# Optimization experiments

Hardware: AMD Instinct MI355X
Metric: run time of the kernel (lower is better)

## Reference

```python
import jax, jax.numpy as jnp
import numpy as np

CHANNELS = 64
HIDDEN = 1024
LAYERS = 24
NODE_TYPES = 19
BN_EPS = 1e-5

N_NODES = 200000
N_EDGES = 800000
N_RULES = 50000


def setup_inputs() -> dict:
    key = jax.random.key(0)
    ks = jax.random.split(key, 16)
    nodes = jax.random.randint(ks[0], (N_NODES,), 0, NODE_TYPES)
    sources = jax.random.randint(ks[1], (N_EDGES,), 0, N_NODES)
    targets = jax.random.randint(ks[2], (N_EDGES,), 0, N_NODES)
    rules = jax.random.randint(ks[3], (N_RULES,), 0, N_NODES)
    f32 = jnp.float32
    emb = jax.random.normal(ks[4], (NODE_TYPES, CHANNELS), f32)
    # per-layer, per-direction (out/back) Conv params, stacked [LAYERS, 2, ...]
    W = jax.random.normal(ks[5], (LAYERS, 2, CHANNELS, CHANNELS), f32) * 0.125  # ~xavier
    b = jax.random.normal(ks[6], (LAYERS, 2, CHANNELS), f32) * 0.01
    gamma = 1.0 + 0.1 * jax.random.normal(ks[7], (LAYERS, 2, CHANNELS), f32)
    beta = 0.01 * jax.random.normal(ks[8], (LAYERS, 2, CHANNELS), f32)
    rmean = 0.01 * jax.random.normal(ks[9], (LAYERS, 2, CHANNELS), f32)
    rvar = jax.random.uniform(ks[10], (LAYERS, 2, CHANNELS), f32, 0.5, 1.5)
    Wh = jax.random.normal(ks[11], (HIDDEN, CHANNELS), f32) * 0.05
    bh = jax.random.normal(ks[12], (HIDDEN,), f32) * 0.01
    Wo = jax.random.normal(ks[13], (1, HIDDEN), f32) * 0.03
    return {"nodes": nodes, "sources": sources, "targets": targets, "rules": rules,
            "emb": emb, "W": W, "b": b, "gamma": gamma, "beta": beta,
            "rmean": rmean, "rvar": rvar, "Wh": Wh, "bh": bh, "Wo": Wo}


def reference(nodes, sources, targets, rules, emb, W, b, gamma, beta, rmean, rvar, Wh, bh, Wo):
    n = nodes.shape[0]

    def conv(x, src, tgt, Wi, bi, g, be, rm, rv):
        # scatter_mean of gathered source features onto target nodes
        s = jax.ops.segment_sum(x[src], tgt, num_segments=n)            # [n, C]
        cnt = jax.ops.segment_sum(jnp.ones(src.shape, x.dtype), tgt, num_segments=n)
        m = s / jnp.maximum(cnt, 1.0)[:, None]
        # eval-mode BatchNorm1d (running stats) fused as affine
        xn = (m - rm) * (g * jax.lax.rsqrt(rv + BN_EPS)) + be
        return jax.nn.relu(xn @ Wi.T + bi)

    def layer(x, p):
        Wl, bl, gl, bel, rml, rvl = p
        out = conv(x, sources, targets, Wl[0], bl[0], gl[0], bel[0], rml[0], rvl[0])
        back = conv(x, targets, sources, Wl[1], bl[1], gl[1], bel[1], rml[1], rvl[1])
        return x + out + back, None

    x = emb[nodes]                                                      # [n, C]
    x, _ = jax.lax.scan(layer, x, (W, b, gamma, beta, rmean, rvar))
    h = jax.nn.relu(x[rules] @ Wh.T + bh)                               # [R, HIDDEN]
    return (h @ Wo.T)[:, 0]                                             # [R]
```

## Files before the change

kernel.cpp:

```cpp
#include <hip/hip_runtime.h>

#define N_NODES 200000
#define N_EDGES 800000
#define N_RULES 50000
#define NLAYERS 24
#define SCAN_NB 196
#define RP_STRIDE 200064

typedef short bf16x8 __attribute__((ext_vector_type(8)));
typedef float floatx4 __attribute__((ext_vector_type(4)));

__device__ __forceinline__ unsigned short f2bf(float f) {
  unsigned int b = __float_as_uint(f);
  b += 0x7FFFu + ((b >> 16) & 1u);
  return (unsigned short)(b >> 16);
}
__device__ __forceinline__ float bf2f(unsigned short u) {
  return __uint_as_float(((unsigned int)u) << 16);
}


__global__ void k_hist(const int* __restrict__ src, const int* __restrict__ tgt,
                       int* __restrict__ deg_out, int* __restrict__ deg_back,
                       int* __restrict__ rank_out, int* __restrict__ rank_back) {
  int e = blockIdx.x * 256 + threadIdx.x;
  rank_out[e]  = atomicAdd(&deg_out[tgt[e]], 1);
  rank_back[e] = atomicAdd(&deg_back[src[e]], 1);
}

__global__ void k_scanA(const int* __restrict__ deg, int* __restrict__ part) {
  int y = blockIdx.y;
  const int* d = deg + y * N_NODES;
  __shared__ int sh[256];
  int t = threadIdx.x;
  int base = blockIdx.x * 1024 + t * 4;
  int s = 0;
  #pragma unroll
  for (int k = 0; k < 4; ++k) { int i = base + k; if (i < N_NODES) s += d[i]; }
  sh[t] = s; __syncthreads();
  for (int off = 128; off > 0; off >>= 1) { if (t < off) sh[t] += sh[t + off]; __syncthreads(); }
  if (t == 0) part[y * SCAN_NB + blockIdx.x] = sh[0];
}

__global__ void k_scanB(int* __restrict__ part, int* __restrict__ rp) {
  int y = blockIdx.y;
  __shared__ int buf[256];
  int t = threadIdx.x;
  int v = (t < SCAN_NB) ? part[y * SCAN_NB + t] : 0;
  buf[t] = v; __syncthreads();
  for (int off = 1; off < 256; off <<= 1) {
    int x = (t >= off) ? buf[t - off] : 0;
    __syncthreads();
    buf[t] += x;
    __syncthreads();
  }
  if (t < SCAN_NB) part[y * SCAN_NB + t] = buf[t] - v;
  if (t == 0) rp[y * RP_STRIDE + N_NODES] = N_EDGES;
}

__global__ void k_scanC(const int* __restrict__ deg, const int* __restrict__ part,
                        int* __restrict__ rp) {
  int y = blockIdx.y;
  const int* d = deg + y * N_NODES;
  int* r = rp + y * RP_STRIDE;
  __shared__ int buf[256];
  int t = threadIdx.x;
  int base = blockIdx.x * 1024 + t * 4;
  int dv[4]; int s = 0;
  #pragma unroll
  for (int k = 0; k < 4; ++k) { int i = base + k; dv[k] = (i < N_NODES) ? d[i] : 0; s += dv[k]; }
  buf[t] = s; __syncthreads();
  int sv = s;
  for (int off = 1; off < 256; off <<= 1) {
    int x = (t >= off) ? buf[t - off] : 0;
    __syncthreads();
    buf[t] += x;
    __syncthreads();
  }
  int e = part[y * SCAN_NB + blockIdx.x] + buf[t] - sv;
  #pragma unroll
  for (int k = 0; k < 4; ++k) { int i = base + k; if (i < N_NODES) r[i] = e; e += dv[k]; }
}

__global__ void k_fill(const int* __restrict__ src, const int* __restrict__ tgt,
                       const int* __restrict__ rp_out, const int* __restrict__ rp_back,
                       const int* __restrict__ rank_out, const int* __restrict__ rank_back,
                       int* __restrict__ ci_out, int* __restrict__ ci_back) {
  int e = blockIdx.x * 256 + threadIdx.x;
  int s = src[e], t = tgt[e];
  ci_out[rp_out[t] + rank_out[e]] = s;
  ci_back[rp_back[s] + rank_back[e]] = t;
}

__global__ void k_prep(const float* __restrict__ W, const float* __restrict__ b,
                       const float* __restrict__ gamma, const float* __restrict__ beta,
                       const float* __restrict__ rmean, const float* __restrict__ rvar,
                       unsigned short* __restrict__ WpF, float* __restrict__ bp) {
  int d = blockIdx.x, l = blockIdx.y, lane = threadIdx.x;
  int ld = l * 2 + d;
  __shared__ float s_s[64], t_s[64];
  float s = gamma[ld * 64 + lane] * rsqrtf(rvar[ld * 64 + lane] + 1e-5f);
  s_s[lane] = s;
  t_s[lane] = beta[ld * 64 + lane] - rmean[ld * 64 + lane] * s;
  __syncthreads();
  float bias = b[ld * 64 + lane];
  for (int j = 0; j < 64; ++j) bias += W[(ld * 64 + lane) * 64 + j] * t_s[j];
  bp[ld * 64 + lane] = bias;
  #pragma unroll
  for (int f = 0; f < 8; ++f) {
    int ct = f >> 1, kh = f & 1;
    int row = ct * 16 + (lane & 15);
    #pragma unroll
    for (int jj = 0; jj < 8; ++jj) {
      int k = kh * 32 + (lane >> 4) * 8 + jj;
      float val = W[(ld * 64 + row) * 64 + k] * s_s[k];
      WpF[(ld * 8 + f) * 512 + lane * 8 + jj] = f2bf(val);
    }
  }
}

__global__ void k_prep2(const float* __restrict__ Wh,
                        unsigned short* __restrict__ WhFhi,
                        unsigned short* __restrict__ WhFlo) {
  int jt = blockIdx.x, lane = threadIdx.x;
  #pragma unroll
  for (int kh = 0; kh < 2; ++kh) {
    #pragma unroll
    for (int jj = 0; jj < 8; ++jj) {
      int j = jt * 16 + (lane & 15);
      int k = kh * 32 + (lane >> 4) * 8 + jj;
      float wv = Wh[j * 64 + k];
      unsigned short hi = f2bf(wv);
      WhFhi[(jt * 2 + kh) * 512 + lane * 8 + jj] = hi;
      WhFlo[(jt * 2 + kh) * 512 + lane * 8 + jj] = f2bf(wv - bf2f(hi));
    }
  }
}

__global__ void k_embed(const int* __restrict__ nodes, const float* __restrict__ emb,
                        unsigned short* __restrict__ hi_a,
                        unsigned short* __restrict__ lo) {
  int gid = blockIdx.x * 256 + threadIdx.x;
  int i = gid >> 6, c = gid & 63;
  float v = emb[nodes[i] * 64 + c];
  unsigned short h = f2bf(v);
  hi_a[gid] = h;
  lo[gid] = f2bf(v - bf2f(h));
}

__global__ __launch_bounds__(256, 8) void k_layer(
    const unsigned short* __restrict__ hi_in,
    unsigned short* __restrict__ hi_out,
    unsigned short* __restrict__ lo,
    const int* __restrict__ rp0, const int* __restrict__ ci0,
    const int* __restrict__ rp1, const int* __restrict__ ci1,
    const unsigned short* __restrict__ WfL, const float* __restrict__ bpL) {
  __shared__ __align__(16) unsigned short m_s[4][2][16 * 72];
  __shared__ float bp_s[128];
  int tid = threadIdx.x, lane = tid & 63, w = tid >> 6;
  if (tid < 128) bp_s[tid] = bpL[tid];
  __syncthreads();
  int base = (blockIdx.x * 4 + w) * 16;
  int n15 = lane & 15, q = lane >> 4;

  int rpv0 = (lane < 17) ? rp0[base + lane] : 0;
  int rpv1 = (lane < 17) ? rp1[base + lane] : 0;
  int rs0 = __builtin_amdgcn_readlane(rpv0, 0);
  int re0 = __builtin_amdgcn_readlane(rpv0, 16);
  int rs1 = __builtin_amdgcn_readlane(rpv1, 0);
  int re1 = __builtin_amdgcn_readlane(rpv1, 16);
  int cv0 = (rs0 + lane < re0) ? ci0[rs0 + lane] : 0;
  int cv1 = (rs1 + lane < re1) ? ci1[rs1 + lane] : 0;

  for (int d = 0; d < 2; ++d) {
    const int* ci = d ? ci1 : ci0;
    int rpv = d ? rpv1 : rpv0;
    int rs  = d ? rs1  : rs0;
    int re  = d ? re1  : re0;
    int cv  = d ? cv1  : cv0;
    unsigned short* md = &m_s[w][d][0];
    int cur = 0;
    int cstart = rs;
    int cend = __builtin_amdgcn_readlane(rpv, 1);
    float acc = 0.f;

    for (int cb = rs; cb < re; cb += 64) {
      int ce = (cb + 64 < re) ? cb + 64 : re;
      int cv_next = (cb + 64 + lane < re) ? ci[cb + 64 + lane] : 0;
      for (int j0 = cb; j0 < ce; j0 += 16) {
        float v[16];
        #pragma unroll
        for (int u = 0; u < 16; ++u) {
          int sn = __builtin_amdgcn_readlane(cv, j0 + u - cb);
          v[u] = bf2f(hi_in[sn * 64 + lane]);
        }
        #pragma unroll
        for (int u = 0; u < 16; ++u) {
          int j = j0 + u;
          if (j < ce) {
            while (j >= cend) {
              int deg = cend - cstart;
              float invc = deg > 0 ? __builtin_amdgcn_rcpf((float)deg) : 0.f;
              md[cur * 72 + lane] = f2bf(acc * invc);
              acc = 0.f; cur++; cstart = cend;
              cend = __builtin_amdgcn_readlane(rpv, cur + 1);
            }
            acc += v[u];
          }
        }
      }
      cv = cv_next;
    }
    #pragma unroll 1
    while (cur < 16) {
      int deg = cend - cstart;
      float invc = deg > 0 ? __builtin_amdgcn_rcpf((float)deg) : 0.f;
      md[cur * 72 + lane] = f2bf(acc * invc);
      acc = 0.f; cstart = cend; cur++;
      if (cur < 16) cend = __builtin_amdgcn_readlane(rpv, cur + 1);
    }
  }

  bf16x8 b0d0 = *(const bf16x8*)&m_s[w][0][n15 * 72 + q * 8];
  bf16x8 b1d0 = *(const bf16x8*)&m_s[w][0][n15 * 72 + 32 + q * 8];
  bf16x8 b0d1 = *(const bf16x8*)&m_s[w][1][n15 * 72 + q * 8];
  bf16x8 b1d1 = *(const bf16x8*)&m_s[w][1][n15 * 72 + 32 + q * 8];
  float* ys = (float*)&m_s[w][0][0];
  #pragma unroll
  for (int ct = 0; ct < 4; ++ct) {
    const unsigned short* wf0 = WfL + (ct * 2) * 512 + lane * 8;
    const unsigned short* wf1 = WfL + 4096 + (ct * 2) * 512 + lane * 8;
    floatx4 d40 = {0.f, 0.f, 0.f, 0.f};
    floatx4 d41 = {0.f, 0.f, 0.f, 0.f};
    d40 = __builtin_amdgcn_mfma_f32_16x16x32_bf16(*(const bf16x8*)wf0, b0d0, d40, 0, 0, 0);
    d40 = __builtin_amdgcn_mfma_f32_16x16x32_bf16(*(const bf16x8*)(wf0 + 512), b1d0, d40, 0, 0, 0);
    d41 = __builtin_amdgcn_mfma_f32_16x16x32_bf16(*(const bf16x8*)wf1, b0d1, d41, 0, 0, 0);
    d41 = __builtin_amdgcn_mfma_f32_16x16x32_bf16(*(const bf16x8*)(wf1 + 512), b1d1, d41, 0, 0, 0);
    int c0 = ct * 16 + q * 4;
    floatx4 yv;
    #pragma unroll
    for (int i = 0; i < 4; ++i)
      yv[i] = fmaxf(d40[i] + bp_s[c0 + i], 0.f)
            + fmaxf(d41[i] + bp_s[64 + c0 + i], 0.f);
    *(floatx4*)&ys[n15 * 68 + c0] = yv;
  }

  #pragma unroll
  for (int r = 0; r < 16; ++r) {
    int gi = (base + r) * 64 + lane;
    float xv = bf2f(hi_in[gi]) + bf2f(lo[gi]) + ys[r * 68 + lane];
    unsigned short h = f2bf(xv);
    hi_out[gi] = h;
    lo[gi] = f2bf(xv - bf2f(h));
  }
}

__global__ __launch_bounds__(256) void k_final(
    const unsigned short* __restrict__ hi, const unsigned short* __restrict__ lo,
    const int* __restrict__ rules,
    const unsigned short* __restrict__ WhFhi, const unsigned short* __restrict__ WhFlo,
    const float* __restrict__ bh, const float* __restrict__ Wo,
    float* __restrict__ out) {
  __shared__ __align__(16) float bh_s[1024], wo_s[1024];
  int tid = threadIdx.x, lane = tid & 63, w = tid >> 6;
  ((floatx4*)bh_s)[tid] = ((const floatx4*)bh)[tid];
  ((floatx4*)wo_s)[tid] = ((const floatx4*)Wo)[tid];
  __syncthreads();
  int n15 = lane & 15, q = lane >> 4;
  int rbase = (blockIdx.x * 4 + w) * 16;
  int ru = rbase + n15;
  int nd = rules[ru < N_RULES ? ru : N_RULES - 1];
  bf16x8 b0h = *(const bf16x8*)&hi[nd * 64 + q * 8];
  bf16x8 b1h = *(const bf16x8*)&hi[nd * 64 + 32 + q * 8];
  bf16x8 b0l = *(const bf16x8*)&lo[nd * 64 + q * 8];
  bf16x8 b1l = *(const bf16x8*)&lo[nd * 64 + 32 + q * 8];
  float acc = 0.f;
  #pragma unroll 4
  for (int jt = 0; jt < 64; ++jt) {
    const unsigned short* fh = WhFhi + (jt * 2) * 512 + lane * 8;
    const unsigned short* fl = WhFlo + (jt * 2) * 512 + lane * 8;
    bf16x8 a0h = *(const bf16x8*)fh;
    bf16x8 a1h = *(const bf16x8*)(fh + 512);
    bf16x8 a0l = *(const bf16x8*)fl;
    bf16x8 a1l = *(const bf16x8*)(fl + 512);
    floatx4 d4 = {0.f, 0.f, 0.f, 0.f};
    d4 = __builtin_amdgcn_mfma_f32_16x16x32_bf16(a0h, b0h, d4, 0, 0, 0);
    d4 = __builtin_amdgcn_mfma_f32_16x16x32_bf16(a1h, b1h, d4, 0, 0, 0);
    d4 = __builtin_amdgcn_mfma_f32_16x16x32_bf16(a0h, b0l, d4, 0, 0, 0);
    d4 = __builtin_amdgcn_mfma_f32_16x16x32_bf16(a1h, b1l, d4, 0, 0, 0);
    d4 = __builtin_amdgcn_mfma_f32_16x16x32_bf16(a0l, b0h, d4, 0, 0, 0);
    d4 = __builtin_amdgcn_mfma_f32_16x16x32_bf16(a1l, b1h, d4, 0, 0, 0);
    floatx4 bh4 = *(const floatx4*)&bh_s[jt * 16 + q * 4];
    floatx4 wo4 = *(const floatx4*)&wo_s[jt * 16 + q * 4];
    #pragma unroll
    for (int i = 0; i < 4; ++i)
      acc += fmaxf(d4[i] + bh4[i], 0.f) * wo4[i];
  }
  acc += __shfl_down(acc, 32);
  acc += __shfl_down(acc, 16);
  if (lane < 16 && rbase + lane < N_RULES) out[rbase + lane] = acc;
}

extern "C" void kernel_launch(void* const* d_in, const int* in_sizes, int n_in,
                              void* d_out, int out_size, void* d_ws, size_t ws_size,
                              hipStream_t stream) {
  const int* nodes = (const int*)d_in[0];
  const int* sources = (const int*)d_in[1];
  const int* targets = (const int*)d_in[2];
  const int* rules = (const int*)d_in[3];
  const float* emb = (const float*)d_in[4];
  const float* W = (const float*)d_in[5];
  const float* b = (const float*)d_in[6];
  const float* gamma = (const float*)d_in[7];
  const float* beta = (const float*)d_in[8];
  const float* rmean = (const float*)d_in[9];
  const float* rvar = (const float*)d_in[10];
  const float* Wh = (const float*)d_in[11];
  const float* bh = (const float*)d_in[12];
  const float* Wo = (const float*)d_in[13];
  float* out = (float*)d_out;

  if (ws_size < 95100000u) return;

  char* ws = (char*)d_ws;
  unsigned short* hi_a = (unsigned short*)(ws + 0);
  unsigned short* hi_b = (unsigned short*)(ws + 25600000);
  unsigned short* lo   = (unsigned short*)(ws + 51200000);
  int* deg_out  = (int*)(ws + 76800000);
  int* deg_back = (int*)(ws + 77600000);
  int* rank_out = (int*)(ws + 78400000);
  int* rank_back= (int*)(ws + 81600000);
  int* rp_out   = (int*)(ws + 84800000);
  int* rp_back  = (int*)(ws + 85600256);
  int* ci_out   = (int*)(ws + 86400512);
  int* ci_back  = (int*)(ws + 89600512);
  int* part     = (int*)(ws + 92800512);
  unsigned short* WpF   = (unsigned short*)(ws + 92802080);
  float* bp             = (float*)(ws + 93195296);
  unsigned short* WhFhi = (unsigned short*)(ws + 93207584);
  unsigned short* WhFlo = (unsigned short*)(ws + 93338656);

  (void)hipMemsetAsync(deg_out, 0, 1600000u, stream);

  k_hist<<<3125, 256, 0, stream>>>(sources, targets, deg_out, deg_back,
                                   rank_out, rank_back);
  k_scanA<<<dim3(SCAN_NB, 2), 256, 0, stream>>>(deg_out, part);
  k_scanB<<<dim3(1, 2), 256, 0, stream>>>(part, rp_out);
  k_scanC<<<dim3(SCAN_NB, 2), 256, 0, stream>>>(deg_out, part, rp_out);
  k_fill<<<3125, 256, 0, stream>>>(sources, targets, rp_out, rp_back,
                                   rank_out, rank_back, ci_out, ci_back);
  k_prep<<<dim3(2, NLAYERS), 64, 0, stream>>>(W, b, gamma, beta, rmean, rvar, WpF, bp);
  k_prep2<<<64, 64, 0, stream>>>(Wh, WhFhi, WhFlo);
  k_embed<<<50000, 256, 0, stream>>>(nodes, emb, hi_a, lo);

  const unsigned short* hin = hi_a;
  unsigned short* hout = hi_b;
  for (int l = 0; l < NLAYERS; ++l) {
    k_layer<<<3125, 256, 0, stream>>>(hin, hout, lo,
                                      rp_out, ci_out, rp_back, ci_back,
                                      WpF + (size_t)l * 8192, bp + (size_t)l * 128);
    const unsigned short* tmp = hin; hin = hout; hout = (unsigned short*)tmp;
  }
  k_final<<<782, 256, 0, stream>>>(hin, lo, rules, WhFhi, WhFlo, bh, Wo, out);
}
```

Baseline: 1.822 ms.

## Interleave out/back edge gathers to double loads in flight per wave

Merges the two sequential direction loops (out and back edges) into one loop that issues both directions' 16-row gathers before accumulating either, and prefetches the next 64 column indices for both up front. The goal is more memory-level parallelism per wave, so each wave has up to 32 independent row loads in flight and gather latency is better hidden. Launch bounds drop from 8 to 6 waves per SIMD to make room for the extra registers, trading occupancy for per-wave parallelism. There is a risk that lower occupancy or register spills offset the gain.

New measurement: 1.495 ms, median of 2. 18.0% less time.

```diff
diff --git a/kernel.cpp b/kernel.cpp
--- a/kernel.cpp
+++ b/kernel.cpp
@@ -148,7 +148,7 @@
   lo[gid] = f2bf(v - bf2f(h));
 }
 
-__global__ __launch_bounds__(256, 8) void k_layer(
+__global__ __launch_bounds__(256, 6) void k_layer(
     const unsigned short* __restrict__ hi_in,
     unsigned short* __restrict__ hi_out,
     unsigned short* __restrict__ lo,
@@ -169,56 +169,94 @@
   int re0 = __builtin_amdgcn_readlane(rpv0, 16);
   int rs1 = __builtin_amdgcn_readlane(rpv1, 0);
   int re1 = __builtin_amdgcn_readlane(rpv1, 16);
-  int cv0 = (rs0 + lane < re0) ? ci0[rs0 + lane] : 0;
-  int cv1 = (rs1 + lane < re1) ? ci1[rs1 + lane] : 0;
-
-  for (int d = 0; d < 2; ++d) {
-    const int* ci = d ? ci1 : ci0;
-    int rpv = d ? rpv1 : rpv0;
-    int rs  = d ? rs1  : rs0;
-    int re  = d ? re1  : re0;
-    int cv  = d ? cv1  : cv0;
-    unsigned short* md = &m_s[w][d][0];
-    int cur = 0;
-    int cstart = rs;
-    int cend = __builtin_amdgcn_readlane(rpv, 1);
-    float acc = 0.f;
-
-    for (int cb = rs; cb < re; cb += 64) {
-      int ce = (cb + 64 < re) ? cb + 64 : re;
-      int cv_next = (cb + 64 + lane < re) ? ci[cb + 64 + lane] : 0;
-      for (int j0 = cb; j0 < ce; j0 += 16) {
-        float v[16];
-        #pragma unroll
-        for (int u = 0; u < 16; ++u) {
-          int sn = __builtin_amdgcn_readlane(cv, j0 + u - cb);
-          v[u] = bf2f(hi_in[sn * 64 + lane]);
-        }
-        #pragma unroll
-        for (int u = 0; u < 16; ++u) {
-          int j = j0 + u;
-          if (j < ce) {
-            while (j >= cend) {
-              int deg = cend - cstart;
-              float invc = deg > 0 ? __builtin_amdgcn_rcpf((float)deg) : 0.f;
-              md[cur * 72 + lane] = f2bf(acc * invc);
-              acc = 0.f; cur++; cstart = cend;
-              cend = __builtin_amdgcn_readlane(rpv, cur + 1);
-            }
-            acc += v[u];
+  int nb0 = re0 - rs0, nb1 = re1 - rs1;
+
+  int cv0  = (lane < nb0)      ? ci0[rs0 + lane]      : 0;
+  int cv1  = (lane < nb1)      ? ci1[rs1 + lane]      : 0;
+  int cv0n = (64 + lane < nb0) ? ci0[rs0 + 64 + lane] : 0;
+  int cv1n = (64 + lane < nb1) ? ci1[rs1 + 64 + lane] : 0;
+
+  int cur0 = 0, cs0 = rs0, ce0 = __builtin_amdgcn_readlane(rpv0, 1);
+  int cur1 = 0, cs1 = rs1, ce1 = __builtin_amdgcn_readlane(rpv1, 1);
+  float a0 = 0.f, a1 = 0.f;
+
+  int g0max = (nb0 + 15) >> 4, g1max = (nb1 + 15) >> 4;
+  int gmax = g0max > g1max ? g0max : g1max;
+
+  for (int g = 0; g < gmax; ++g) {
+    int off = g << 4;
+    int boff = off & 63;
+    if (g && boff == 0) {
+      cv0 = cv0n; cv1 = cv1n;
+      cv0n = (off + 64 + lane < nb0) ? ci0[rs0 + off + 64 + lane] : 0;
+      cv1n = (off + 64 + lane < nb1) ? ci1[rs1 + off + 64 + lane] : 0;
+    }
+    bool do0 = off < nb0, do1 = off < nb1;
+    float v0[16], v1[16];
+    if (do0) {
+      #pragma unroll
+      for (int u = 0; u < 16; ++u) {
+        int sn = __builtin_amdgcn_readlane(cv0, boff + u);
+        v0[u] = bf2f(hi_in[sn * 64 + lane]);
+      }
+    }
+    if (do1) {
+      #pragma unroll
+      for (int u = 0; u < 16; ++u) {
+        int sn = __builtin_amdgcn_readlane(cv1, boff + u);
+        v1[u] = bf2f(hi_in[sn * 64 + lane]);
+      }
+    }
+    if (do0) {
+      int jb = rs0 + off;
+      #pragma unroll
+      for (int u = 0; u < 16; ++u) {
+        int j = jb + u;
+        if (j < re0) {
+          while (j >= ce0) {
+            int deg = ce0 - cs0;
+            float invc = deg > 0 ? __builtin_amdgcn_rcpf((float)deg) : 0.f;
+            m_s[w][0][cur0 * 72 + lane] = f2bf(a0 * invc);
+            a0 = 0.f; cur0++; cs0 = ce0;
+            ce0 = __builtin_amdgcn_readlane(rpv0, cur0 + 1);
           }
+          a0 += v0[u];
         }
       }
-      cv = cv_next;
-    }
-    #pragma unroll 1
-    while (cur < 16) {
-      int deg = cend - cstart;
-      float invc = deg > 0 ? __builtin_amdgcn_rcpf((float)deg) : 0.f;
-      md[cur * 72 + lane] = f2bf(acc * invc);
-      acc = 0.f; cstart = cend; cur++;
-      if (cur < 16) cend = __builtin_amdgcn_readlane(rpv, cur + 1);
-    }
+    }
+    if (do1) {
+      int jb = rs1 + off;
+      #pragma unroll
+      for (int u = 0; u < 16; ++u) {
+        int j = jb + u;
+        if (j < re1) {
+          while (j >= ce1) {
+            int deg = ce1 - cs1;
+            float invc = deg > 0 ? __builtin_amdgcn_rcpf((float)deg) : 0.f;
+            m_s[w][1][cur1 * 72 + lane] = f2bf(a1 * invc);
+            a1 = 0.f; cur1++; cs1 = ce1;
+            ce1 = __builtin_amdgcn_readlane(rpv1, cur1 + 1);
+          }
+          a1 += v1[u];
+        }
+      }
+    }
+  }
+  #pragma unroll 1
+  while (cur0 < 16) {
+    int deg = ce0 - cs0;
+    float invc = deg > 0 ? __builtin_amdgcn_rcpf((float)deg) : 0.f;
+    m_s[w][0][cur0 * 72 + lane] = f2bf(a0 * invc);
+    a0 = 0.f; cs0 = ce0; cur0++;
+    if (cur0 < 16) ce0 = __builtin_amdgcn_readlane(rpv0, cur0 + 1);
+  }
+  #pragma unroll 1
+  while (cur1 < 16) {
+    int deg = ce1 - cs1;
+    float invc = deg > 0 ? __builtin_amdgcn_rcpf((float)deg) : 0.f;
+    m_s[w][1][cur1 * 72 + lane] = f2bf(a1 * invc);
+    a1 = 0.f; cs1 = ce1; cur1++;
+    if (cur1 < 16) ce1 = __builtin_amdgcn_readlane(rpv1, cur1 + 1);
   }
 
   bf16x8 b0d0 = *(const bf16x8*)&m_s[w][0][n15 * 72 + q * 8];
```

## Interleave four independent gather streams per wave in layer aggregation

Applied to the files above, without the earlier changes.

The per-wave CSR gather is rewritten so the two directions, each split into two halves of 8 target nodes, run as four interleaved streams. Each iteration issues 64 gathered loads before any accumulation, and the index chunks for the next 64 edges are prefetched. The aim is more memory-level parallelism to hide gather latency. In exchange it uses more registers, and launch bounds drop from 8 to 4 waves per SIMD, which reduces occupancy.

After: 1.917 ms. 5.2% more time.

```diff
diff --git a/kernel.cpp b/kernel.cpp
--- a/kernel.cpp
+++ b/kernel.cpp
@@ -148,7 +148,7 @@
   lo[gid] = f2bf(v - bf2f(h));
 }
 
-__global__ __launch_bounds__(256, 8) void k_layer(
+__global__ __launch_bounds__(256, 4) void k_layer(
     const unsigned short* __restrict__ hi_in,
     unsigned short* __restrict__ hi_out,
     unsigned short* __restrict__ lo,
@@ -166,60 +166,104 @@
   int rpv0 = (lane < 17) ? rp0[base + lane] : 0;
   int rpv1 = (lane < 17) ? rp1[base + lane] : 0;
   int rs0 = __builtin_amdgcn_readlane(rpv0, 0);
+  int rm0 = __builtin_amdgcn_readlane(rpv0, 8);
   int re0 = __builtin_amdgcn_readlane(rpv0, 16);
   int rs1 = __builtin_amdgcn_readlane(rpv1, 0);
+  int rm1 = __builtin_amdgcn_readlane(rpv1, 8);
   int re1 = __builtin_amdgcn_readlane(rpv1, 16);
-  int cv0 = (rs0 + lane < re0) ? ci0[rs0 + lane] : 0;
-  int cv1 = (rs1 + lane < re1) ? ci1[rs1 + lane] : 0;
-
-  for (int d = 0; d < 2; ++d) {
-    const int* ci = d ? ci1 : ci0;
-    int rpv = d ? rpv1 : rpv0;
-    int rs  = d ? rs1  : rs0;
-    int re  = d ? re1  : re0;
-    int cv  = d ? cv1  : cv0;
-    unsigned short* md = &m_s[w][d][0];
-    int cur = 0;
-    int cstart = rs;
-    int cend = __builtin_amdgcn_readlane(rpv, 1);
-    float acc = 0.f;
-
-    for (int cb = rs; cb < re; cb += 64) {
-      int ce = (cb + 64 < re) ? cb + 64 : re;
-      int cv_next = (cb + 64 + lane < re) ? ci[cb + 64 + lane] : 0;
-      for (int j0 = cb; j0 < ce; j0 += 16) {
-        float v[16];
-        #pragma unroll
-        for (int u = 0; u < 16; ++u) {
-          int sn = __builtin_amdgcn_readlane(cv, j0 + u - cb);
-          v[u] = bf2f(hi_in[sn * 64 + lane]);
-        }
-        #pragma unroll
-        for (int u = 0; u < 16; ++u) {
-          int j = j0 + u;
-          if (j < ce) {
-            while (j >= cend) {
-              int deg = cend - cstart;
-              float invc = deg > 0 ? __builtin_amdgcn_rcpf((float)deg) : 0.f;
-              md[cur * 72 + lane] = f2bf(acc * invc);
-              acc = 0.f; cur++; cstart = cend;
-              cend = __builtin_amdgcn_readlane(rpv, cur + 1);
-            }
-            acc += v[u];
-          }
-        }
-      }
-      cv = cv_next;
+  int nbA0 = rm0 - rs0, nbB0 = re0 - rm0;
+  int nbA1 = rm1 - rs1, nbB1 = re1 - rm1;
+
+  int cvA0  = (lane < nbA0)      ? ci0[rs0 + lane]      : 0;
+  int cvB0  = (lane < nbB0)      ? ci0[rm0 + lane]      : 0;
+  int cvA1  = (lane < nbA1)      ? ci1[rs1 + lane]      : 0;
+  int cvB1  = (lane < nbB1)      ? ci1[rm1 + lane]      : 0;
+  int cvnA0 = (64 + lane < nbA0) ? ci0[rs0 + 64 + lane] : 0;
+  int cvnB0 = (64 + lane < nbB0) ? ci0[rm0 + 64 + lane] : 0;
+  int cvnA1 = (64 + lane < nbA1) ? ci1[rs1 + 64 + lane] : 0;
+  int cvnB1 = (64 + lane < nbB1) ? ci1[rm1 + 64 + lane] : 0;
+
+  int curA0 = 0, csA0 = rs0, ceA0 = __builtin_amdgcn_readlane(rpv0, 1);
+  int curB0 = 8, csB0 = rm0, ceB0 = __builtin_amdgcn_readlane(rpv0, 9);
+  int curA1 = 0, csA1 = rs1, ceA1 = __builtin_amdgcn_readlane(rpv1, 1);
+  int curB1 = 8, csB1 = rm1, ceB1 = __builtin_amdgcn_readlane(rpv1, 9);
+  float aA0 = 0.f, aB0 = 0.f, aA1 = 0.f, aB1 = 0.f;
+
+  int gm0 = (nbA0 + 15) >> 4, gm1 = (nbB0 + 15) >> 4;
+  int gm2 = (nbA1 + 15) >> 4, gm3 = (nbB1 + 15) >> 4;
+  int gmax = gm0 > gm1 ? gm0 : gm1;
+  if (gm2 > gmax) gmax = gm2;
+  if (gm3 > gmax) gmax = gm3;
+
+#define ISSUE(V, cv, nbS)                                                 \
+  { int off_ = g << 4;                                                    \
+    if (off_ < nbS) {                                                     \
+      int boff_ = off_ & 63;                                              \
+      _Pragma("unroll")                                                   \
+      for (int u = 0; u < 16; ++u) {                                      \
+        int sn = __builtin_amdgcn_readlane(cv, boff_ + u);                \
+        const unsigned short* p = hi_in + sn * 64;                        \
+        V[u] = bf2f(p[lane]);                                             \
+      } } }
+
+#define ROLLS(cv, cvn, ci, rsS, nbS)                                      \
+  { cv = cvn;                                                             \
+    int ob_ = (g << 4) + 64;                                              \
+    cvn = (ob_ + lane < nbS) ? ci[rsS + ob_ + lane] : 0; }
+
+#define ACCS(V, dirIdx, rpv, rsS, reS, nbS, cur, cs, ce, acc)             \
+  { int off_ = g << 4;                                                    \
+    if (off_ < nbS) {                                                     \
+      int jb = rsS + off_;                                                \
+      _Pragma("unroll")                                                   \
+      for (int u = 0; u < 16; ++u) {                                      \
+        int j = jb + u;                                                   \
+        if (j < reS) {                                                    \
+          while (j >= ce) {                                               \
+            int deg = ce - cs;                                            \
+            float invc = deg > 0 ? __builtin_amdgcn_rcpf((float)deg) : 0.f;\
+            m_s[w][dirIdx][cur * 72 + lane] = f2bf(acc * invc);           \
+            acc = 0.f; cur++; cs = ce;                                    \
+            ce = __builtin_amdgcn_readlane(rpv, cur + 1);                 \
+          }                                                               \
+          acc += V[u];                                                    \
+        } } } }
+
+  float v0[16], v1[16], v2[16], v3[16];
+  for (int g = 0; g < gmax; ++g) {
+    if (g && ((g & 3) == 0)) {
+      ROLLS(cvA0, cvnA0, ci0, rs0, nbA0)
+      ROLLS(cvB0, cvnB0, ci0, rm0, nbB0)
+      ROLLS(cvA1, cvnA1, ci1, rs1, nbA1)
+      ROLLS(cvB1, cvnB1, ci1, rm1, nbB1)
     }
-    #pragma unroll 1
-    while (cur < 16) {
-      int deg = cend - cstart;
-      float invc = deg > 0 ? __builtin_amdgcn_rcpf((float)deg) : 0.f;
-      md[cur * 72 + lane] = f2bf(acc * invc);
-      acc = 0.f; cstart = cend; cur++;
-      if (cur < 16) cend = __builtin_amdgcn_readlane(rpv, cur + 1);
-    }
-  }
+    ISSUE(v0, cvA0, nbA0)
+    ISSUE(v1, cvB0, nbB0)
+    ISSUE(v2, cvA1, nbA1)
+    ISSUE(v3, cvB1, nbB1)
+    ACCS(v0, 0, rpv0, rs0, rm0, nbA0, curA0, csA0, ceA0, aA0)
+    ACCS(v1, 0, rpv0, rm0, re0, nbB0, curB0, csB0, ceB0, aB0)
+    ACCS(v2, 1, rpv1, rs1, rm1, nbA1, curA1, csA1, ceA1, aA1)
+    ACCS(v3, 1, rpv1, rm1, re1, nbB1, curB1, csB1, ceB1, aB1)
+  }
+#undef ISSUE
+#undef ROLLS
+#undef ACCS
+
+#define TAIL(dirIdx, rpv, cur, cs, ce, acc, lim)                          \
+  _Pragma("unroll 1")                                                     \
+  while (cur < lim) {                                                     \
+    int deg = ce - cs;                                                    \
+    float invc = deg > 0 ? __builtin_amdgcn_rcpf((float)deg) : 0.f;       \
+    m_s[w][dirIdx][cur * 72 + lane] = f2bf(acc * invc);                   \
+    acc = 0.f; cs = ce; cur++;                                            \
+    if (cur < lim) ce = __builtin_amdgcn_readlane(rpv, cur + 1);          \
+  }
+  TAIL(0, rpv0, curA0, csA0, ceA0, aA0, 8)
+  TAIL(0, rpv0, curB0, csB0, ceB0, aB0, 16)
+  TAIL(1, rpv1, curA1, csA1, ceA1, aA1, 8)
+  TAIL(1, rpv1, curB1, csB1, ceB1, aB1, 16)
+#undef TAIL
 
   bf16x8 b0d0 = *(const bf16x8*)&m_s[w][0][n15 * 72 + q * 8];
   bf16x8 b1d0 = *(const bf16x8*)&m_s[w][0][n15 * 72 + 32 + q * 8];
```
